# Kernel optimization log

Hardware: AMD Instinct MI355X
Metric: run time of the kernel (lower is better)

## Reference

```python
import jax, jax.numpy as jnp
import numpy as np

# dims
V, D, H = 30000, 300, 300
NS, L = 10000, 32
B, NMAX, MMAX = 256, 128, 128
EPS = 0.1          # sinkhorn entropic regularizer
ITERS = 50         # fixed sinkhorn sweeps (replaces convergence check, jit-friendly)
NEG = 1e9
PAD = 0


def setup_inputs() -> dict:
    key = jax.random.key(0)
    ks = jax.random.split(key, 12)
    data = jax.random.randint(ks[0], (NS, L), 0, V, dtype=jnp.int32)
    row_idx = jax.random.randint(ks[1], (B, NMAX), 0, NS, dtype=jnp.int32)
    col_idx = jax.random.randint(ks[2], (B, MMAX), 0, NS, dtype=jnp.int32)
    row_len = jax.random.randint(ks[3], (B,), 1, NMAX + 1, dtype=jnp.int32)
    col_len = jax.random.randint(ks[4], (B,), 1, MMAX + 1, dtype=jnp.int32)
    g = lambda k, shape, fan: (jax.random.normal(k, shape, jnp.float32) / np.sqrt(fan)).astype(jnp.float32)
    return {
        'data': data, 'row_idx': row_idx, 'col_idx': col_idx,
        'row_len': row_len, 'col_len': col_len,
        'emb': g(ks[5], (V, D), D),
        'W1': g(ks[6], (D, H), D), 'b1': jnp.zeros((H,), jnp.float32),
        'W2': g(ks[7], (H, H), H), 'b2': jnp.zeros((H,), jnp.float32),
        'Wc': g(ks[8], (2 * H, H), 2 * H), 'bc': jnp.zeros((H,), jnp.float32),
        'Wcls': g(ks[9], (2 * H, H), 2 * H), 'bcls': jnp.zeros((H,), jnp.float32),
        'Wout': g(ks[10], (H, 2), H), 'bout': jnp.zeros((2,), jnp.float32),
    }


def _forward(data, row_idx, col_idx, row_len, col_len,
             emb, W1, b1, W2, b2, Wc, bc, Wcls, bcls, Wout, bout):
    # ---- Embedder: token embedding + masked mean pool over tokens ----
    tok = emb[data]                                        # [NS, L, D]
    tmask = (data != PAD).astype(tok.dtype)[..., None]     # [NS, L, 1]
    enc = (tok * tmask).sum(1) / jnp.clip(tmask.sum(1), 1.0)   # [NS, D]
    # ---- attention_forward: 2-layer FFN ----
    henc = jax.nn.relu(jax.nn.relu(enc @ W1 + b1) @ W2 + b2)   # [NS, H]
    # ---- variable-length gather + pad (scope) ----
    rows = henc[row_idx]                                   # [B, NMAX, H]
    cols = henc[col_idx]                                   # [B, MMAX, H]
    rmask = (jnp.arange(NMAX)[None, :] < row_len[:, None]).astype(henc.dtype)
    cmask = (jnp.arange(MMAX)[None, :] < col_len[:, None]).astype(henc.dtype)
    rows = rows * rmask[..., None]
    cols = cols * cmask[..., None]
    # ---- batched pairwise cosine cost ----
    rn = rows / (jnp.linalg.norm(rows, axis=-1, keepdims=True) + 1e-8)
    cn = cols / (jnp.linalg.norm(cols, axis=-1, keepdims=True) + 1e-8)
    C = 1.0 - jnp.einsum('bnd,bmd->bnm', rn, cn)           # [B, NMAX, MMAX]
    pmask = rmask[:, :, None] * cmask[:, None, :]
    Cm = jnp.where(pmask > 0, C, 1e4)
    # uniform marginals over valid rows/cols (log-domain, -inf -> -NEG on pads)
    loga = jnp.where(rmask > 0, -jnp.log(row_len.astype(C.dtype))[:, None], -NEG)
    logb = jnp.where(cmask > 0, -jnp.log(col_len.astype(C.dtype))[:, None], -NEG)
    # ---- log-domain Sinkhorn (row/col marginal rescaling) ----
    def step(carry, _):
        f, g = carry
        f = EPS * loga - EPS * jax.nn.logsumexp((g[:, None, :] - Cm) / EPS, axis=2)
        g = EPS * logb - EPS * jax.nn.logsumexp((f[:, :, None] - Cm) / EPS, axis=1)
        return (f, g), None
    (f, g), _ = jax.lax.scan(step, (jnp.zeros_like(loga), jnp.zeros_like(logb)), None, length=ITERS)
    P = jnp.exp((f[:, :, None] + g[:, None, :] - Cm) / EPS) * pmask  # [B, NMAX, MMAX]
    # ---- attend: column_alignments @ rows, row_alignments @ columns ----
    attended_row = jnp.einsum('bnm,bnd->bmd', P, rows)     # P^T @ rows
    attended_col = jnp.einsum('bnm,bmd->bnd', P, cols)     # P @ cols
    # ---- compare_forward (1 layer) + masked sum ----
    cr = jax.nn.relu(jnp.concatenate([rows, attended_col], -1) @ Wc + bc)
    cr = (cr * rmask[..., None]).sum(1)                    # [B, H]
    cc = jax.nn.relu(jnp.concatenate([cols, attended_row], -1) @ Wc + bc)
    cc = (cc * cmask[..., None]).sum(1)                    # [B, H]
    # ---- cls_forward + out ----
    z = jax.nn.relu(jnp.concatenate([cr, cc], -1) @ Wcls + bcls)
    return z @ Wout + bout                                 # [B, 2]


def reference(data, row_idx, col_idx, row_len, col_len,
              emb, W1, b1, W2, b2, Wc, bc, Wcls, bcls, Wout, bout):
    return _forward(data, row_idx, col_idx, row_len, col_len,
                    emb, W1, b1, W2, b2, Wc, bc, Wcls, bcls, Wout, bout)
```

## Files before the change

kernel.cpp:

```cpp
#include <hip/hip_runtime.h>
#include <math.h>

#define NS 10000
#define LSEQ 32
#define DDIM 300
#define HDIM 300
#define BB 256
#define NMAX 128
#define MMAX 128
#define EPSR 0.1f
#define SITERS 50
#define KPAD 320

typedef __attribute__((ext_vector_type(8))) short bf16x8;
typedef __attribute__((ext_vector_type(4))) float f32x4;

__device__ __forceinline__ ushort f2bf(float x) {
  union { float f; unsigned u; } c; c.f = x;
  unsigned r = (c.u + 0x7fffu + ((c.u >> 16) & 1u)) >> 16;
  return (ushort)r;
}
__device__ __forceinline__ float bf2f(ushort h) {
  union { unsigned u; float f; } c; c.u = ((unsigned)h) << 16;
  return c.f;
}

__global__ __launch_bounds__(256) void k_embed(const int* __restrict__ data,
                                               const float* __restrict__ emb,
                                               ushort* __restrict__ enchi,
                                               ushort* __restrict__ enclo) {
  __shared__ int ids[LSEQ];
  __shared__ __align__(16) float4 part[3][76];
  int s = blockIdx.x;
  int tid = threadIdx.x;
  if (tid < LSEQ) ids[tid] = data[s * LSEQ + tid];
  __syncthreads();
  int cnt = 0;
#pragma unroll
  for (int t = 0; t < LSEQ; ++t) cnt += (ids[t] != 0) ? 1 : 0;
  int g = tid / 75, d = tid - g * 75;
  const float4* emb4 = (const float4*)emb;
  if (g < 3) {
    float4 acc = make_float4(0.f, 0.f, 0.f, 0.f);
    for (int t = g; t < LSEQ; t += 3) {
      int id = ids[t];
      if (id != 0) {
        float4 e = emb4[(size_t)id * 75 + d];
        acc.x += e.x; acc.y += e.y; acc.z += e.z; acc.w += e.w;
      }
    }
    part[g][d] = acc;
  }
  __syncthreads();
  if (g == 0) {
    float4 a = part[0][d], b = part[1][d], c = part[2][d];
    float inv = 1.f / (float)(cnt > 0 ? cnt : 1);
    float v[4] = {(a.x + b.x + c.x) * inv, (a.y + b.y + c.y) * inv,
                  (a.z + b.z + c.z) * inv, (a.w + b.w + c.w) * inv};
    ushort4 h, l;
    h.x = f2bf(v[0]); l.x = f2bf(v[0] - bf2f(h.x));
    h.y = f2bf(v[1]); l.y = f2bf(v[1] - bf2f(h.y));
    h.z = f2bf(v[2]); l.z = f2bf(v[2] - bf2f(h.z));
    h.w = f2bf(v[3]); l.w = f2bf(v[3] - bf2f(h.w));
    *(ushort4*)&enchi[(size_t)s * KPAD + d * 4] = h;
    *(ushort4*)&enclo[(size_t)s * KPAD + d * 4] = l;
  } else if (g == 1 && d < 5) {
    ushort4 z; z.x = z.y = z.z = z.w = 0;
    *(ushort4*)&enchi[(size_t)s * KPAD + 300 + d * 4] = z;
    *(ushort4*)&enclo[(size_t)s * KPAD + 300 + d * 4] = z;
  }
}

__global__ __launch_bounds__(256) void k_cvtw(const float* __restrict__ W,
                                              ushort* __restrict__ hiT,
                                              ushort* __restrict__ loT,
                                              int K, int N, int Npad) {
  int idx = blockIdx.x * 256 + threadIdx.x;
  if (idx >= Npad * KPAD) return;
  int n = idx / KPAD, k = idx - n * KPAD;
  float v = (n < N && k < K) ? W[(size_t)k * N + n] : 0.f;
  ushort h = f2bf(v);
  hiT[idx] = h;
  loT[idx] = f2bf(v - bf2f(h));
}

__global__ __launch_bounds__(256) void k_cvtwc(const float* __restrict__ Wc,
                                               ushort* __restrict__ hiT,
                                               ushort* __restrict__ loT) {
  int idx = blockIdx.x * 256 + threadIdx.x;
  if (idx >= 640 * KPAD) return;
  int n = idx / KPAD, k = idx - n * KPAD;
  float v = 0.f;
  if (k < 300 && n < 600)
    v = (n < 300) ? Wc[(size_t)k * 300 + n]
                  : Wc[(size_t)(300 + k) * 300 + (n - 300)];
  ushort h = f2bf(v);
  hiT[idx] = h;
  loT[idx] = f2bf(v - bf2f(h));
}

__global__ __launch_bounds__(256) void k_gemm_mfma(
    const ushort* __restrict__ Ahi, const ushort* __restrict__ Alo,
    const ushort* __restrict__ BhiT, const ushort* __restrict__ BloT,
    const float* __restrict__ bias, int M, int N, int relu,
    float* __restrict__ Cf, ushort* __restrict__ Chi,
    ushort* __restrict__ Clo) {
  __shared__ ushort lds[4][64][40];
  int tid = threadIdx.x;
  int m0 = blockIdx.x * 64, n0 = blockIdx.y * 64;
  int row = tid >> 2, ch = tid & 3;
  bool mok = (m0 + row) < M;
  const ushort* pAh = Ahi + (size_t)(m0 + row) * KPAD + ch * 8;
  const ushort* pAl = Alo + (size_t)(m0 + row) * KPAD + ch * 8;
  const ushort* pBh = BhiT + (size_t)(n0 + row) * KPAD + ch * 8;
  const ushort* pBl = BloT + (size_t)(n0 + row) * KPAD + ch * 8;
  uint4 rAh, rAl, rBh, rBl;
  uint4 z4; z4.x = z4.y = z4.z = z4.w = 0;
  auto ld = [&](int c) {
    int o = c * 32;
    rAh = mok ? *(const uint4*)(pAh + o) : z4;
    rAl = mok ? *(const uint4*)(pAl + o) : z4;
    rBh = *(const uint4*)(pBh + o);
    rBl = *(const uint4*)(pBl + o);
  };
  auto st = [&]() {
    *(uint4*)&lds[0][row][ch * 8] = rAh;
    *(uint4*)&lds[1][row][ch * 8] = rAl;
    *(uint4*)&lds[2][row][ch * 8] = rBh;
    *(uint4*)&lds[3][row][ch * 8] = rBl;
  };
  int w = tid >> 6, lane = tid & 63;
  int q = lane >> 4, l16 = lane & 15;
  int arow = w * 16 + l16;
  f32x4 acc[4] = {{0.f, 0.f, 0.f, 0.f}, {0.f, 0.f, 0.f, 0.f},
                  {0.f, 0.f, 0.f, 0.f}, {0.f, 0.f, 0.f, 0.f}};
  ld(0); st(); __syncthreads();
  for (int c = 0; c < 10; ++c) {
    if (c < 9) ld(c + 1);
    bf16x8 ah = *(const bf16x8*)&lds[0][arow][q * 8];
    bf16x8 al = *(const bf16x8*)&lds[1][arow][q * 8];
#pragma unroll
    for (int t = 0; t < 4; ++t) {
      int brow = t * 16 + l16;
      bf16x8 bh = *(const bf16x8*)&lds[2][brow][q * 8];
      bf16x8 bl = *(const bf16x8*)&lds[3][brow][q * 8];
      acc[t] = __builtin_amdgcn_mfma_f32_16x16x32_bf16(ah, bh, acc[t], 0, 0, 0);
      acc[t] = __builtin_amdgcn_mfma_f32_16x16x32_bf16(ah, bl, acc[t], 0, 0, 0);
      acc[t] = __builtin_amdgcn_mfma_f32_16x16x32_bf16(al, bh, acc[t], 0, 0, 0);
    }
    __syncthreads();
    if (c < 9) st();
    __syncthreads();
  }
#pragma unroll
  for (int t = 0; t < 4; ++t) {
    int n = n0 + t * 16 + l16;
    bool nin = n < N;
    float bz = (bias && nin) ? bias[n] : 0.f;
#pragma unroll
    for (int r = 0; r < 4; ++r) {
      int m = m0 + w * 16 + q * 4 + r;
      if (m >= M) continue;
      float v = acc[t][r] + bz;
      if (relu) v = v > 0.f ? v : 0.f;
      if (Cf && nin) Cf[(size_t)m * N + n] = v;
      if (Chi) {
        ushort h = 0, l = 0;
        if (nin) { h = f2bf(v); l = f2bf(v - bf2f(h)); }
        Chi[(size_t)m * KPAD + n] = h;
        Clo[(size_t)m * KPAD + n] = l;
      }
    }
  }
}

__global__ __launch_bounds__(256) void k_rnorm(const float* __restrict__ henc,
                                               float* __restrict__ rinv) {
  int s = blockIdx.x * 4 + (threadIdx.x >> 6);
  int lane = threadIdx.x & 63;
  if (s >= NS) return;
  const float* src = henc + (size_t)s * HDIM;
  float ss = 0.f;
#pragma unroll
  for (int q = 0; q < 5; ++q) {
    int d = lane + q * 64;
    float x = (d < HDIM) ? src[d] : 0.f;
    ss += x * x;
  }
#pragma unroll
  for (int off = 32; off > 0; off >>= 1) ss += __shfl_down(ss, off, 64);
  if (lane == 0) rinv[s] = 1.f / (sqrtf(ss) + 1e-8f);
}

__global__ __launch_bounds__(512) void k_cost(
    const float* __restrict__ henc, const float* __restrict__ rinv,
    const int* __restrict__ ridx, const int* __restrict__ cidx,
    const int* __restrict__ rlen, const int* __restrict__ clen,
    float* __restrict__ Kmat) {
  int b = blockIdx.z;
  int r0 = blockIdx.x * 64, c0 = blockIdx.y * 64;
  int rl = rlen[b], cl = clen[b];
  float* Kg = Kmat + (size_t)b * NMAX * MMAX;
  int tid = threadIdx.x;
  if (r0 >= rl || c0 >= cl) {
    for (int l = tid; l < 64 * 16; l += 512) {
      int i = l >> 4, j = (l & 15) << 2;
      *(float4*)&Kg[(size_t)(r0 + i) * MMAX + c0 + j] =
          make_float4(0.f, 0.f, 0.f, 0.f);
    }
    return;
  }
  __shared__ int rix[64], cix[64];
  __shared__ float rnv[64], cnv[64];
  __shared__ __align__(16) float smem[2][2][2][16][68];
  float* red = &smem[0][0][0][0][0];
  int half = tid >> 8, t = tid & 255, tx = t & 15, ty = t >> 4;
  if (tid < 64) {
    int r = ridx[b * NMAX + r0 + tid];
    rix[tid] = r; rnv[tid] = rinv[r];
  } else if (tid < 128) {
    int r = cidx[b * MMAX + c0 + tid - 64];
    cix[tid - 64] = r; cnv[tid - 64] = rinv[r];
  }
  __syncthreads();
  int kbase = half * 160;
  int rowT = t >> 2, kq = t & 3;
  const float* aPtr = henc + (size_t)rix[rowT] * HDIM + kbase + kq * 4;
  const float* bPtr = henc + (size_t)cix[rowT] * HDIM + kbase + kq * 4;
  float aS = rnv[rowT], cS = cnv[rowT];
  float aR[4], bR[4];
  auto loadC = [&](int c) {
    int k = kbase + c * 16 + kq * 4;
    if (k + 3 < HDIM) {
      float4 a4 = *(const float4*)(aPtr + c * 16);
      float4 b4 = *(const float4*)(bPtr + c * 16);
      aR[0] = a4.x * aS; aR[1] = a4.y * aS; aR[2] = a4.z * aS; aR[3] = a4.w * aS;
      bR[0] = b4.x * cS; bR[1] = b4.y * cS; bR[2] = b4.z * cS; bR[3] = b4.w * cS;
    } else {
#pragma unroll
      for (int i = 0; i < 4; ++i) {
        bool ok = (k + i) < HDIM;
        aR[i] = ok ? aPtr[c * 16 + i] * aS : 0.f;
        bR[i] = ok ? bPtr[c * 16 + i] * cS : 0.f;
      }
    }
  };
  auto storeC = [&](int buf) {
#pragma unroll
    for (int i = 0; i < 4; ++i) smem[buf][half][0][kq * 4 + i][rowT] = aR[i];
#pragma unroll
    for (int i = 0; i < 4; ++i) smem[buf][half][1][kq * 4 + i][rowT] = bR[i];
  };
  float acc[4][4] = {};
  loadC(0);
  storeC(0);
  __syncthreads();
  int cur = 0;
  for (int c = 0; c < 10; ++c) {
    if (c < 9) loadC(c + 1);
#pragma unroll
    for (int kk = 0; kk < 16; ++kk) {
      float4 av = *(const float4*)&smem[cur][half][0][kk][ty * 4];
      float4 bv = *(const float4*)&smem[cur][half][1][kk][tx * 4];
      float a[4] = {av.x, av.y, av.z, av.w};
      float w[4] = {bv.x, bv.y, bv.z, bv.w};
#pragma unroll
      for (int i = 0; i < 4; ++i)
#pragma unroll
        for (int j = 0; j < 4; ++j) acc[i][j] += a[i] * w[j];
    }
    if (c < 9) storeC(cur ^ 1);
    __syncthreads();
    cur ^= 1;
  }
  if (half == 1) {
#pragma unroll
    for (int i = 0; i < 4; ++i)
#pragma unroll
      for (int j = 0; j < 4; ++j) red[(i * 4 + j) * 256 + t] = acc[i][j];
  }
  __syncthreads();
  if (half == 0) {
#pragma unroll
    for (int i = 0; i < 4; ++i)
#pragma unroll
      for (int j = 0; j < 4; ++j) acc[i][j] += red[(i * 4 + j) * 256 + t];
#pragma unroll
    for (int i = 0; i < 4; ++i) {
      int n = r0 + ty * 4 + i;
      float4 kv;
      float* kvp = &kv.x;
#pragma unroll
      for (int j = 0; j < 4; ++j) {
        int m = c0 + tx * 4 + j;
        kvp[j] = (n < rl && m < cl) ? expf((acc[i][j] - 1.f) / EPSR) : 0.f;
      }
      *(float4*)&Kg[(size_t)n * MMAX + c0 + tx * 4] = kv;
    }
  }
}

__global__ __launch_bounds__(512) void k_sinkhorn(
    float* __restrict__ Kmat, const int* __restrict__ rlen,
    const int* __restrict__ clen) {
  __shared__ __align__(16) float vq[4][36];
  __shared__ __align__(16) float uq[4][36];
  int b = blockIdx.x;
  int tid = threadIdx.x;
  int n = tid >> 2, q = tid & 3;
  int rl = rlen[b], cl = clen[b];
  float* Kg = Kmat + (size_t)b * NMAX * MMAX;
  float kr[32], kt[32];
  const float4* Kg4 = (const float4*)(Kg + (size_t)n * MMAX + 32 * q);
#pragma unroll
  for (int t = 0; t < 8; ++t) *(float4*)&kr[4 * t] = Kg4[t];
#pragma unroll
  for (int j = 0; j < 32; ++j) kt[j] = Kg[(size_t)(32 * q + j) * MMAX + n];
  if (tid < 128) vq[tid >> 5][tid & 31] = (tid < cl) ? 1.f : 0.f;
  float av = (n < rl) ? 1.f / (float)rl : 0.f;
  float bv = (n < cl) ? 1.f / (float)cl : 0.f;
  float un = 0.f;
  __syncthreads();
  for (int it = 0; it < SITERS; ++it) {
    float s = 0.f;
#pragma unroll
    for (int t = 0; t < 8; ++t) {
      float4 vv = *(const float4*)&vq[q][4 * t];
      s += kr[4 * t + 0] * vv.x + kr[4 * t + 1] * vv.y +
           kr[4 * t + 2] * vv.z + kr[4 * t + 3] * vv.w;
    }
    s += __shfl_xor(s, 1, 64);
    s += __shfl_xor(s, 2, 64);
    un = (n < rl) ? av / s : 0.f;
    if (q == 0) uq[n >> 5][n & 31] = un;
    __syncthreads();
    float s2 = 0.f;
#pragma unroll
    for (int t = 0; t < 8; ++t) {
      float4 uu = *(const float4*)&uq[q][4 * t];
      s2 += kt[4 * t + 0] * uu.x + kt[4 * t + 1] * uu.y +
            kt[4 * t + 2] * uu.z + kt[4 * t + 3] * uu.w;
    }
    s2 += __shfl_xor(s2, 1, 64);
    s2 += __shfl_xor(s2, 2, 64);
    float vm = (n < cl) ? bv / s2 : 0.f;
    if (q == 0) vq[n >> 5][n & 31] = vm;
    __syncthreads();
  }
  float4* Pg4 = (float4*)(Kg + (size_t)n * MMAX + 32 * q);
#pragma unroll
  for (int t = 0; t < 8; ++t) {
    float4 vv = *(const float4*)&vq[q][4 * t];
    float4 p;
    p.x = un * kr[4 * t + 0] * vv.x;
    p.y = un * kr[4 * t + 1] * vv.y;
    p.z = un * kr[4 * t + 2] * vv.z;
    p.w = un * kr[4 * t + 3] * vv.w;
    Pg4[t] = p;
  }
}

template <int SIDE>
__global__ __launch_bounds__(256) void k_att_cmp(
    const float* __restrict__ P, const float* __restrict__ HcB,
    const int* __restrict__ idx_main, const int* __restrict__ idx_other,
    const int* __restrict__ len_main, const int* __restrict__ len_other,
    const float* __restrict__ bc, float* __restrict__ outacc) {
  int b = blockIdx.y;
  int c0 = blockIdx.x * 64;
  int lm = len_main[b], lo = len_other[b];
  __shared__ __align__(16) float smem[2][2][16][68];
  __shared__ int iox[NMAX];
  __shared__ int imx[NMAX];
  int tid = threadIdx.x, tx = tid & 15, ty = tid >> 4;
  int jj = tid & 63, kq = tid >> 6;
  if (tid < 128) iox[tid] = idx_other[b * NMAX + tid];
  else imx[tid - 128] = idx_main[b * NMAX + tid - 128];
  __syncthreads();
  const float* Pb = P + (size_t)b * NMAX * MMAX;
  bool cok = (c0 + jj) < HDIM;
  int nkc = (lo + 15) >> 4;
  int nmt = (lm + 63) >> 6;
  float pR[4], gR[4];
  auto loadPG = [&](int mt, int kc) {
    int m0 = mt * 64, k0 = kc * 16;
    if (SIDE == 0) {
#pragma unroll
      for (int p = 0; p < 4; ++p)
        pR[p] = Pb[(size_t)(m0 + ty + p * 16) * MMAX + k0 + tx];
    } else {
#pragma unroll
      for (int p = 0; p < 4; ++p)
        pR[p] = Pb[(size_t)(k0 + kq + p * 4) * MMAX + m0 + jj];
    }
#pragma unroll
    for (int p = 0; p < 4; ++p) {
      int row = iox[k0 + kq + p * 4];
      gR[p] = cok ? HcB[(size_t)row * 600 + 300 + c0 + jj] : 0.f;
    }
  };
  auto storePG = [&](int buf) {
    if (SIDE == 0) {
#pragma unroll
      for (int p = 0; p < 4; ++p) smem[buf][0][tx][ty + p * 16] = pR[p];
    } else {
#pragma unroll
      for (int p = 0; p < 4; ++p) smem[buf][0][kq + p * 4][jj] = pR[p];
    }
#pragma unroll
    for (int p = 0; p < 4; ++p) smem[buf][1][kq + p * 4][jj] = gR[p];
  };
  float colsum[4] = {0.f, 0.f, 0.f, 0.f};
  loadPG(0, 0);
  storePG(0);
  __syncthreads();
  int cur = 0;
  for (int mt = 0; mt < nmt; ++mt) {
    float acc[4][4] = {};
    for (int kc = 0; kc < nkc; ++kc) {
      bool last = (mt == nmt - 1) && (kc == nkc - 1);
      if (!last) {
        int nm = (kc + 1 < nkc) ? mt : mt + 1;
        int nk = (kc + 1 < nkc) ? kc + 1 : 0;
        loadPG(nm, nk);
      }
#pragma unroll
      for (int kk = 0; kk < 16; ++kk) {
        float4 av = *(const float4*)&smem[cur][0][kk][ty * 4];
        float4 gv = *(const float4*)&smem[cur][1][kk][tx * 4];
        float a[4] = {av.x, av.y, av.z, av.w};
        float g[4] = {gv.x, gv.y, gv.z, gv.w};
#pragma unroll
        for (int i = 0; i < 4; ++i)
#pragma unroll
          for (int j = 0; j < 4; ++j) acc[i][j] += a[i] * g[j];
      }
      if (!last) storePG(cur ^ 1);
      __syncthreads();
      cur ^= 1;
    }
#pragma unroll
    for (int i = 0; i < 4; ++i) {
      int mi = mt * 64 + ty * 4 + i;
      if (mi >= lm) continue;
      int hrow = imx[mi];
#pragma unroll
      for (int j = 0; j < 4; ++j) {
        int col = c0 + tx * 4 + j;
        if (col >= HDIM) continue;
        float y = acc[i][j] + HcB[(size_t)hrow * 600 + col] + bc[col];
        colsum[j] += y > 0.f ? y : 0.f;
      }
    }
  }
  __syncthreads();
  float(*red)[68] = (float(*)[68]) & smem[0][0][0][0];
#pragma unroll
  for (int j = 0; j < 4; ++j) red[ty][tx * 4 + j] = colsum[j];
  __syncthreads();
  if (tid < 64) {
    float s = 0.f;
#pragma unroll
    for (int r = 0; r < 16; ++r) s += red[r][tid];
    int col = c0 + tid;
    if (col < HDIM) outacc[(size_t)b * HDIM + col] = s;
  }
}

__global__ __launch_bounds__(320) void k_cls(
    const float* __restrict__ cr, const float* __restrict__ cc,
    const float* __restrict__ Wcls, const float* __restrict__ bcls,
    const float* __restrict__ Wout, const float* __restrict__ bout,
    float* __restrict__ out) {
  __shared__ __align__(16) float cz[2 * HDIM];
  __shared__ float zz[HDIM];
  int b = blockIdx.x, tid = threadIdx.x;
  if (tid < HDIM) {
    cz[tid] = cr[(size_t)b * HDIM + tid];
    cz[HDIM + tid] = cc[(size_t)b * HDIM + tid];
  }
  __syncthreads();
  if (tid < HDIM) {
    float acc = bcls[tid];
    for (int k4 = 0; k4 < 2 * HDIM; k4 += 4) {
      float4 c = *(const float4*)&cz[k4];
      acc += c.x * Wcls[(size_t)(k4 + 0) * HDIM + tid] +
             c.y * Wcls[(size_t)(k4 + 1) * HDIM + tid] +
             c.z * Wcls[(size_t)(k4 + 2) * HDIM + tid] +
             c.w * Wcls[(size_t)(k4 + 3) * HDIM + tid];
    }
    zz[tid] = acc > 0.f ? acc : 0.f;
  }
  __syncthreads();
  int o = tid >> 6, lane = tid & 63;
  if (o < 2) {
    float p = 0.f;
    for (int j = lane; j < HDIM; j += 64) p += zz[j] * Wout[(size_t)j * 2 + o];
#pragma unroll
    for (int off = 32; off > 0; off >>= 1) p += __shfl_down(p, off, 64);
    if (lane == 0) out[b * 2 + o] = p + bout[o];
  }
}

extern "C" void kernel_launch(void* const* d_in, const int* in_sizes, int n_in,
                              void* d_out, int out_size, void* d_ws, size_t ws_size,
                              hipStream_t stream) {
  (void)in_sizes; (void)n_in; (void)out_size; (void)ws_size;
  const int* data = (const int*)d_in[0];
  const int* row_idx = (const int*)d_in[1];
  const int* col_idx = (const int*)d_in[2];
  const int* row_len = (const int*)d_in[3];
  const int* col_len = (const int*)d_in[4];
  const float* emb = (const float*)d_in[5];
  const float* W1 = (const float*)d_in[6];
  const float* b1 = (const float*)d_in[7];
  const float* W2 = (const float*)d_in[8];
  const float* b2 = (const float*)d_in[9];
  const float* Wc = (const float*)d_in[10];
  const float* bc = (const float*)d_in[11];
  const float* Wcls = (const float*)d_in[12];
  const float* bcls = (const float*)d_in[13];
  const float* Wout = (const float*)d_in[14];
  const float* bout = (const float*)d_in[15];
  float* out = (float*)d_out;

  char* wp = (char*)d_ws;
  auto carve = [&](size_t bytes) {
    char* p = wp; wp += (bytes + 255) & ~(size_t)255; return p;
  };
  ushort* enchi = (ushort*)carve((size_t)NS * KPAD * 2);
  ushort* enclo = (ushort*)carve((size_t)NS * KPAD * 2);
  ushort* h1hi = (ushort*)carve((size_t)NS * KPAD * 2);
  ushort* h1lo = (ushort*)carve((size_t)NS * KPAD * 2);
  ushort* hehi = (ushort*)carve((size_t)NS * KPAD * 2);
  ushort* helo = (ushort*)carve((size_t)NS * KPAD * 2);
  float* henc = (float*)carve((size_t)NS * HDIM * 4);
  ushort* W1hi = (ushort*)carve((size_t)KPAD * KPAD * 2);
  ushort* W1lo = (ushort*)carve((size_t)KPAD * KPAD * 2);
  ushort* W2hi = (ushort*)carve((size_t)KPAD * KPAD * 2);
  ushort* W2lo = (ushort*)carve((size_t)KPAD * KPAD * 2);
  ushort* Wchi = (ushort*)carve((size_t)640 * KPAD * 2);
  ushort* Wclo = (ushort*)carve((size_t)640 * KPAD * 2);
  float* HcB = (float*)carve((size_t)NS * 600 * 4);
  float* Km = (float*)carve((size_t)BB * NMAX * MMAX * 4);
  float* rinv = (float*)carve((size_t)NS * 4);
  float* cr = (float*)carve((size_t)BB * HDIM * 4);
  float* cc = (float*)carve((size_t)BB * HDIM * 4);

  int gM = (NS + 63) / 64;

  k_embed<<<NS, 256, 0, stream>>>(data, emb, enchi, enclo);
  k_cvtw<<<(KPAD * KPAD + 255) / 256, 256, 0, stream>>>(W1, W1hi, W1lo, DDIM,
                                                        HDIM, KPAD);
  k_cvtw<<<(KPAD * KPAD + 255) / 256, 256, 0, stream>>>(W2, W2hi, W2lo, HDIM,
                                                        HDIM, KPAD);
  k_cvtwc<<<(640 * KPAD + 255) / 256, 256, 0, stream>>>(Wc, Wchi, Wclo);
  k_gemm_mfma<<<dim3(gM, 5), 256, 0, stream>>>(
      enchi, enclo, W1hi, W1lo, b1, NS, HDIM, 1, nullptr, h1hi, h1lo);
  k_gemm_mfma<<<dim3(gM, 5), 256, 0, stream>>>(
      h1hi, h1lo, W2hi, W2lo, b2, NS, HDIM, 1, henc, hehi, helo);
  k_rnorm<<<(NS + 3) / 4, 256, 0, stream>>>(henc, rinv);
  k_gemm_mfma<<<dim3(gM, 10), 256, 0, stream>>>(
      hehi, helo, Wchi, Wclo, nullptr, NS, 2 * HDIM, 0, HcB, nullptr, nullptr);
  k_cost<<<dim3(2, 2, BB), 512, 0, stream>>>(henc, rinv, row_idx, col_idx,
                                             row_len, col_len, Km);
  k_sinkhorn<<<BB, 512, 0, stream>>>(Km, row_len, col_len);
  k_att_cmp<0><<<dim3(5, BB), 256, 0, stream>>>(
      Km, HcB, row_idx, col_idx, row_len, col_len, bc, cr);
  k_att_cmp<1><<<dim3(5, BB), 256, 0, stream>>>(
      Km, HcB, col_idx, row_idx, col_len, row_len, bc, cc);
  k_cls<<<BB, 320, 0, stream>>>(cr, cc, Wcls, bcls, Wout, bout, out);
}
```

Before: 449.8 us.

## Compute cosine cost matrix with split-bf16 MFMA on pre-normalized embeddings

Replaces the FP32 FMA tiled cost kernel with an MFMA kernel that takes hi/lo bf16 split operands and uses three products per tile to keep near-fp32 accuracy. A new normalize-and-split kernel builds unit-norm hi/lo copies of the hidden encodings, so the cost kernel no longer applies per-row scaling. The fp32 henc output of the second GEMM and the rinv buffer are dropped. This moves the per-pair dot products onto matrix cores at the cost of an extra normalization pass and slightly different rounding, which the exp with 1/EPS amplifies.

```diff
diff --git a/kernel.cpp b/kernel.cpp
--- a/kernel.cpp
+++ b/kernel.cpp
@@ -105,7 +105,7 @@
     const float* __restrict__ bias, int M, int N, int relu,
     float* __restrict__ Cf, ushort* __restrict__ Chi,
     ushort* __restrict__ Clo) {
-  __shared__ ushort lds[4][64][40];
+  __shared__ __align__(16) ushort lds[4][64][40];
   int tid = threadIdx.x;
   int m0 = blockIdx.x * 64, n0 = blockIdx.y * 64;
   int row = tid >> 2, ch = tid & 3;
@@ -174,26 +174,40 @@
   }
 }
 
-__global__ __launch_bounds__(256) void k_rnorm(const float* __restrict__ henc,
-                                               float* __restrict__ rinv) {
+__global__ __launch_bounds__(256) void k_norm_split(
+    const ushort* __restrict__ hehi, const ushort* __restrict__ helo,
+    ushort* __restrict__ hnhi, ushort* __restrict__ hnlo) {
   int s = blockIdx.x * 4 + (threadIdx.x >> 6);
   int lane = threadIdx.x & 63;
   if (s >= NS) return;
-  const float* src = henc + (size_t)s * HDIM;
+  const ushort* ph = hehi + (size_t)s * KPAD;
+  const ushort* pl = helo + (size_t)s * KPAD;
+  float x[5];
   float ss = 0.f;
 #pragma unroll
   for (int q = 0; q < 5; ++q) {
     int d = lane + q * 64;
-    float x = (d < HDIM) ? src[d] : 0.f;
-    ss += x * x;
+    x[q] = bf2f(ph[d]) + bf2f(pl[d]);
+    ss += x[q] * x[q];
   }
 #pragma unroll
   for (int off = 32; off > 0; off >>= 1) ss += __shfl_down(ss, off, 64);
-  if (lane == 0) rinv[s] = 1.f / (sqrtf(ss) + 1e-8f);
-}
-
-__global__ __launch_bounds__(512) void k_cost(
-    const float* __restrict__ henc, const float* __restrict__ rinv,
+  ss = __shfl(ss, 0, 64);
+  float inv = 1.f / (sqrtf(ss) + 1e-8f);
+  ushort* qh = hnhi + (size_t)s * KPAD;
+  ushort* ql = hnlo + (size_t)s * KPAD;
+#pragma unroll
+  for (int q = 0; q < 5; ++q) {
+    int d = lane + q * 64;
+    float v = x[q] * inv;
+    ushort h = f2bf(v);
+    qh[d] = h;
+    ql[d] = f2bf(v - bf2f(h));
+  }
+}
+
+__global__ __launch_bounds__(256) void k_cost_mfma(
+    const ushort* __restrict__ hnhi, const ushort* __restrict__ hnlo,
     const int* __restrict__ ridx, const int* __restrict__ cidx,
     const int* __restrict__ rlen, const int* __restrict__ clen,
     float* __restrict__ Kmat) {
@@ -203,7 +217,7 @@
   float* Kg = Kmat + (size_t)b * NMAX * MMAX;
   int tid = threadIdx.x;
   if (r0 >= rl || c0 >= cl) {
-    for (int l = tid; l < 64 * 16; l += 512) {
+    for (int l = tid; l < 64 * 16; l += 256) {
       int i = l >> 4, j = (l & 15) << 2;
       *(float4*)&Kg[(size_t)(r0 + i) * MMAX + c0 + j] =
           make_float4(0.f, 0.f, 0.f, 0.f);
@@ -211,91 +225,60 @@
     return;
   }
   __shared__ int rix[64], cix[64];
-  __shared__ float rnv[64], cnv[64];
-  __shared__ __align__(16) float smem[2][2][2][16][68];
-  float* red = &smem[0][0][0][0][0];
-  int half = tid >> 8, t = tid & 255, tx = t & 15, ty = t >> 4;
-  if (tid < 64) {
-    int r = ridx[b * NMAX + r0 + tid];
-    rix[tid] = r; rnv[tid] = rinv[r];
-  } else if (tid < 128) {
-    int r = cidx[b * MMAX + c0 + tid - 64];
-    cix[tid - 64] = r; cnv[tid - 64] = rinv[r];
-  }
-  __syncthreads();
-  int kbase = half * 160;
-  int rowT = t >> 2, kq = t & 3;
-  const float* aPtr = henc + (size_t)rix[rowT] * HDIM + kbase + kq * 4;
-  const float* bPtr = henc + (size_t)cix[rowT] * HDIM + kbase + kq * 4;
-  float aS = rnv[rowT], cS = cnv[rowT];
-  float aR[4], bR[4];
-  auto loadC = [&](int c) {
-    int k = kbase + c * 16 + kq * 4;
-    if (k + 3 < HDIM) {
-      float4 a4 = *(const float4*)(aPtr + c * 16);
-      float4 b4 = *(const float4*)(bPtr + c * 16);
-      aR[0] = a4.x * aS; aR[1] = a4.y * aS; aR[2] = a4.z * aS; aR[3] = a4.w * aS;
-      bR[0] = b4.x * cS; bR[1] = b4.y * cS; bR[2] = b4.z * cS; bR[3] = b4.w * cS;
-    } else {
-#pragma unroll
-      for (int i = 0; i < 4; ++i) {
-        bool ok = (k + i) < HDIM;
-        aR[i] = ok ? aPtr[c * 16 + i] * aS : 0.f;
-        bR[i] = ok ? bPtr[c * 16 + i] * cS : 0.f;
-      }
-    }
-  };
-  auto storeC = [&](int buf) {
-#pragma unroll
-    for (int i = 0; i < 4; ++i) smem[buf][half][0][kq * 4 + i][rowT] = aR[i];
-#pragma unroll
-    for (int i = 0; i < 4; ++i) smem[buf][half][1][kq * 4 + i][rowT] = bR[i];
-  };
-  float acc[4][4] = {};
-  loadC(0);
-  storeC(0);
-  __syncthreads();
-  int cur = 0;
+  __shared__ __align__(16) ushort lds[4][64][40];
+  if (tid < 64) rix[tid] = ridx[b * NMAX + r0 + tid];
+  else if (tid < 128) cix[tid - 64] = cidx[b * MMAX + c0 + tid - 64];
+  __syncthreads();
+  int row = tid >> 2, ch = tid & 3;
+  const ushort* pRh = hnhi + (size_t)rix[row] * KPAD + ch * 8;
+  const ushort* pRl = hnlo + (size_t)rix[row] * KPAD + ch * 8;
+  const ushort* pCh = hnhi + (size_t)cix[row] * KPAD + ch * 8;
+  const ushort* pCl = hnlo + (size_t)cix[row] * KPAD + ch * 8;
+  uint4 rRh, rRl, rCh, rCl;
+  auto ld = [&](int c) {
+    int o = c * 32;
+    rRh = *(const uint4*)(pRh + o);
+    rRl = *(const uint4*)(pRl + o);
+    rCh = *(const uint4*)(pCh + o);
+    rCl = *(const uint4*)(pCl + o);
+  };
+  auto st = [&]() {
+    *(uint4*)&lds[0][row][ch * 8] = rRh;
+    *(uint4*)&lds[1][row][ch * 8] = rRl;
+    *(uint4*)&lds[2][row][ch * 8] = rCh;
+    *(uint4*)&lds[3][row][ch * 8] = rCl;
+  };
+  int w = tid >> 6, lane = tid & 63;
+  int q = lane >> 4, l16 = lane & 15;
+  int arow = w * 16 + l16;
+  f32x4 acc[4] = {{0.f, 0.f, 0.f, 0.f}, {0.f, 0.f, 0.f, 0.f},
+                  {0.f, 0.f, 0.f, 0.f}, {0.f, 0.f, 0.f, 0.f}};
+  ld(0); st(); __syncthreads();
   for (int c = 0; c < 10; ++c) {
-    if (c < 9) loadC(c + 1);
-#pragma unroll
-    for (int kk = 0; kk < 16; ++kk) {
-      float4 av = *(const float4*)&smem[cur][half][0][kk][ty * 4];
-      float4 bv = *(const float4*)&smem[cur][half][1][kk][tx * 4];
-      float a[4] = {av.x, av.y, av.z, av.w};
-      float w[4] = {bv.x, bv.y, bv.z, bv.w};
-#pragma unroll
-      for (int i = 0; i < 4; ++i)
-#pragma unroll
-        for (int j = 0; j < 4; ++j) acc[i][j] += a[i] * w[j];
-    }
-    if (c < 9) storeC(cur ^ 1);
+    if (c < 9) ld(c + 1);
+    bf16x8 ah = *(const bf16x8*)&lds[0][arow][q * 8];
+    bf16x8 al = *(const bf16x8*)&lds[1][arow][q * 8];
+#pragma unroll
+    for (int t = 0; t < 4; ++t) {
+      int brow = t * 16 + l16;
+      bf16x8 bh = *(const bf16x8*)&lds[2][brow][q * 8];
+      bf16x8 bl = *(const bf16x8*)&lds[3][brow][q * 8];
+      acc[t] = __builtin_amdgcn_mfma_f32_16x16x32_bf16(ah, bh, acc[t], 0, 0, 0);
+      acc[t] = __builtin_amdgcn_mfma_f32_16x16x32_bf16(ah, bl, acc[t], 0, 0, 0);
+      acc[t] = __builtin_amdgcn_mfma_f32_16x16x32_bf16(al, bh, acc[t], 0, 0, 0);
+    }
     __syncthreads();
-    cur ^= 1;
-  }
-  if (half == 1) {
-#pragma unroll
-    for (int i = 0; i < 4; ++i)
-#pragma unroll
-      for (int j = 0; j < 4; ++j) red[(i * 4 + j) * 256 + t] = acc[i][j];
-  }
-  __syncthreads();
-  if (half == 0) {
-#pragma unroll
-    for (int i = 0; i < 4; ++i)
-#pragma unroll
-      for (int j = 0; j < 4; ++j) acc[i][j] += red[(i * 4 + j) * 256 + t];
-#pragma unroll
-    for (int i = 0; i < 4; ++i) {
-      int n = r0 + ty * 4 + i;
-      float4 kv;
-      float* kvp = &kv.x;
-#pragma unroll
-      for (int j = 0; j < 4; ++j) {
-        int m = c0 + tx * 4 + j;
-        kvp[j] = (n < rl && m < cl) ? expf((acc[i][j] - 1.f) / EPSR) : 0.f;
-      }
-      *(float4*)&Kg[(size_t)n * MMAX + c0 + tx * 4] = kv;
+    if (c < 9) st();
+    __syncthreads();
+  }
+#pragma unroll
+  for (int t = 0; t < 4; ++t) {
+    int n = c0 + t * 16 + l16;
+#pragma unroll
+    for (int r = 0; r < 4; ++r) {
+      int m = r0 + w * 16 + q * 4 + r;
+      float kv = (m < rl && n < cl) ? expf((acc[t][r] - 1.f) / EPSR) : 0.f;
+      Kg[(size_t)m * MMAX + n] = kv;
     }
   }
 }
@@ -534,7 +517,8 @@
   ushort* h1lo = (ushort*)carve((size_t)NS * KPAD * 2);
   ushort* hehi = (ushort*)carve((size_t)NS * KPAD * 2);
   ushort* helo = (ushort*)carve((size_t)NS * KPAD * 2);
-  float* henc = (float*)carve((size_t)NS * HDIM * 4);
+  ushort* hnhi = (ushort*)carve((size_t)NS * KPAD * 2);
+  ushort* hnlo = (ushort*)carve((size_t)NS * KPAD * 2);
   ushort* W1hi = (ushort*)carve((size_t)KPAD * KPAD * 2);
   ushort* W1lo = (ushort*)carve((size_t)KPAD * KPAD * 2);
   ushort* W2hi = (ushort*)carve((size_t)KPAD * KPAD * 2);
@@ -543,7 +527,6 @@
   ushort* Wclo = (ushort*)carve((size_t)640 * KPAD * 2);
   float* HcB = (float*)carve((size_t)NS * 600 * 4);
   float* Km = (float*)carve((size_t)BB * NMAX * MMAX * 4);
-  float* rinv = (float*)carve((size_t)NS * 4);
   float* cr = (float*)carve((size_t)BB * HDIM * 4);
   float* cc = (float*)carve((size_t)BB * HDIM * 4);
 
@@ -558,12 +541,12 @@
   k_gemm_mfma<<<dim3(gM, 5), 256, 0, stream>>>(
       enchi, enclo, W1hi, W1lo, b1, NS, HDIM, 1, nullptr, h1hi, h1lo);
   k_gemm_mfma<<<dim3(gM, 5), 256, 0, stream>>>(
-      h1hi, h1lo, W2hi, W2lo, b2, NS, HDIM, 1, henc, hehi, helo);
-  k_rnorm<<<(NS + 3) / 4, 256, 0, stream>>>(henc, rinv);
+      h1hi, h1lo, W2hi, W2lo, b2, NS, HDIM, 1, nullptr, hehi, helo);
+  k_norm_split<<<(NS + 3) / 4, 256, 0, stream>>>(hehi, helo, hnhi, hnlo);
   k_gemm_mfma<<<dim3(gM, 10), 256, 0, stream>>>(
       hehi, helo, Wchi, Wclo, nullptr, NS, 2 * HDIM, 0, HcB, nullptr, nullptr);
-  k_cost<<<dim3(2, 2, BB), 512, 0, stream>>>(henc, rinv, row_idx, col_idx,
-                                             row_len, col_len, Km);
+  k_cost_mfma<<<dim3(2, 2, BB), 256, 0, stream>>>(hnhi, hnlo, row_idx, col_idx,
+                                                  row_len, col_len, Km);
   k_sinkhorn<<<BB, 512, 0, stream>>>(Km, row_len, col_len);
   k_att_cmp<0><<<dim3(5, BB), 256, 0, stream>>>(
       Km, HcB, row_idx, col_idx, row_len, col_len, bc, cr);
```

Result: faster. 428.3 us (-4.8%).
